# Optimization experiments

Hardware: AMD Instinct MI355X
Metric: run time of the kernel (lower is better)

Reference implementation:

```python
import jax, jax.numpy as jnp
import numpy as np

HEAD_NUM = 4
B, S, D = 8, 1024, 512


def setup_inputs() -> dict:
    k = jax.random.key(0)
    kq, kk, kv = jax.random.split(k, 3)
    return {
        "query": jax.random.normal(kq, (B, S, D), dtype=jnp.float32),
        "key": jax.random.normal(kk, (B, S, D), dtype=jnp.float32),
        "value": jax.random.normal(kv, (B, S, D), dtype=jnp.float32),
    }


def _corr_attention(q, k, v):
    # q,k,v: [B, H, S, hd]
    score = jnp.einsum('bhqd,bhkd->bhqk', q, k)  # raw dot products
    len_q = jnp.sqrt(jnp.sum(q * q, axis=-1))    # [B,H,S]
    len_k = jnp.sqrt(jnp.sum(k * k, axis=-1))    # [B,H,S]
    score = score / (len_q[..., :, None] * len_k[..., None, :])  # cosine similarity
    signal = jnp.sign(score)
    flat = jnp.abs(score).reshape(-1)            # global flatten across B,H,S,S
    n = flat.shape[0]
    idx = jnp.argsort(-flat)                     # descending sort indices
    prob = (jnp.arange(n, dtype=flat.dtype) + 1.0) / n  # (1/n, 2/n, ..., 1)
    ranked = flat.at[idx].set(prob)              # rank-transform: largest -> smallest prob
    score = (-jnp.log(ranked)).reshape(signal.shape) * signal
    return jnp.einsum('bhqk,bhkd->bhqd', score, v)


def reference(query, key, value):
    b, s, d = query.shape
    h = HEAD_NUM
    q = query.reshape(b, s, h, -1).transpose(0, 2, 1, 3)
    k = key.reshape(b, s, h, -1).transpose(0, 2, 1, 3)
    v = value.reshape(b, s, h, -1).transpose(0, 2, 1, 3)
    out = _corr_attention(q, k, v)               # [B,H,S,hd]
    return out.transpose(0, 2, 1, 3).reshape(b, s, d)
```

## Files before the change

kernel.cpp:

```cpp
#include <hip/hip_runtime.h>
#include <math.h>

#define BB 8
#define SS 1024
#define DD 512
#define HH 4
#define HD 128
#define N_SC (BB*HH*SS*SS)

#define NB 8192
#define BINS 13107.2f
#define NBLK 2048
#define NP2 32

#define OFF_S     0
#define SZ_S      ((size_t)N_SC*2)
#define OFF_QN    (OFF_S + SZ_S)
#define SZ_QN     ((size_t)BB*SS*DD*2)
#define OFF_KN    (OFF_QN + SZ_QN)
#define OFF_VT    (OFF_KN + SZ_QN)
#define OFF_PARTS (OFF_VT + SZ_QN)
#define SZ_PARTS  ((size_t)NBLK*(NB/4)*4)
#define OFF_WMAG  (OFF_PARTS + SZ_PARTS)
#define OFF_PART2 (OFF_WMAG + (size_t)NB*2)

typedef __bf16 bf16x8 __attribute__((ext_vector_type(8)));
typedef float  f32x4  __attribute__((ext_vector_type(4)));
typedef unsigned short ushort_t;

__device__ __forceinline__ unsigned bf16rne(float x) {
  unsigned b = __float_as_uint(x);
  return (b + 0x7FFFu + ((b >> 16) & 1u)) >> 16;
}
__device__ __forceinline__ unsigned sbin(float s) {
  return (unsigned)fminf(fabsf(s)*BINS, 8191.0f);
}

__global__ __launch_bounds__(256) void prep_vt_kernel(
    const float* __restrict__ q, const float* __restrict__ k,
    const float* __restrict__ v,
    unsigned* __restrict__ qn, unsigned* __restrict__ kn,
    unsigned* __restrict__ vt) {
  __shared__ float T[64][65];
  int t = threadIdx.x;
  if (blockIdx.x < 16384) {
    int lane = t & 63;
    int row = blockIdx.x*4 + (t >> 6);
    const float* src; unsigned* dst; int r;
    if (row < 32768) { src = q; dst = qn; r = row; }
    else             { src = k; dst = kn; r = row - 32768; }
    int b = r >> 12, s = (r >> 2) & 1023, h = r & 3;
    float2 vv = *(const float2*)(src + ((size_t)(b*1024 + s))*512 + h*128 + lane*2);
    float sum = vv.x*vv.x + vv.y*vv.y;
    #pragma unroll
    for (int off = 32; off; off >>= 1) sum += __shfl_xor(sum, off, 64);
    float inv = rsqrtf(sum);
    unsigned u = bf16rne(vv.x*inv) | (bf16rne(vv.y*inv) << 16);
    dst[(size_t)((b*4 + h)*1024 + s)*64 + lane] = u;
  } else {
    int vb = blockIdx.x - 16384;
    int s0 = (vb & 15)*64, d0 = ((vb >> 4) & 1)*64, bh = vb >> 5;
    int b = bh >> 2, h = bh & 3;
    #pragma unroll
    for (int i = 0; i < 16; i++) {
      int idx = t + i*256, rs = idx >> 6, cd = idx & 63;
      T[rs][cd] = v[((size_t)(b*1024 + s0 + rs))*512 + h*128 + d0 + cd];
    }
    __syncthreads();
    #pragma unroll
    for (int i = 0; i < 8; i++) {
      int idx = t + i*256, rd = idx >> 5, c2 = (idx & 31)*2;
      unsigned u = bf16rne(T[c2][rd]) | (bf16rne(T[c2+1][rd]) << 16);
      vt[(size_t)(bh*128 + d0 + rd)*512 + (s0 + c2)/2] = u;
    }
  }
}

__global__ __launch_bounds__(256) void scores_hist_kernel(
    const ushort_t* __restrict__ qn, const ushort_t* __restrict__ kn,
    ushort_t* __restrict__ S, unsigned* __restrict__ parts) {
  __shared__ ushort_t Qs[128*128];
  __shared__ ushort_t Ks[128*128];
  __shared__ unsigned h8[NB/4];
  int t = threadIdx.x;
  int L = blockIdx.x;
  int bh = L & 31, tile = L >> 5;
  int sq0 = (tile >> 3)*128, sk0 = (tile & 7)*128;

  #pragma unroll
  for (int i = 0; i < 8; i++) h8[t + i*256] = 0;

  const uint4* qg = (const uint4*)qn + (size_t)(bh*1024 + sq0)*16;
  const uint4* kg = (const uint4*)kn + (size_t)(bh*1024 + sk0)*16;
  #pragma unroll
  for (int i = 0; i < 8; i++) {
    int idx = t + i*256, row = idx >> 4, g = idx & 15;
    int sw = g ^ (row & 15);
    *(uint4*)&Qs[row*128 + sw*8] = qg[row*16 + g];
    *(uint4*)&Ks[row*128 + sw*8] = kg[row*16 + g];
  }
  __syncthreads();

  int w = t >> 6, lane = t & 63, m16 = lane & 15, q2 = lane >> 4;
  int wm = (w >> 1)*64, wn = (w & 1)*64;
  f32x4 acc[4][4];
  #pragma unroll
  for (int i = 0; i < 4; i++)
    #pragma unroll
    for (int j = 0; j < 4; j++) acc[i][j] = (f32x4){0.f,0.f,0.f,0.f};

  #pragma unroll
  for (int ks = 0; ks < 4; ks++) {
    int sw = ((ks*4 + q2) ^ m16)*8;
    bf16x8 a[4], bb[4];
    #pragma unroll
    for (int i = 0; i < 4; i++) a[i]  = *(const bf16x8*)&Qs[(wm + i*16 + m16)*128 + sw];
    #pragma unroll
    for (int j = 0; j < 4; j++) bb[j] = *(const bf16x8*)&Ks[(wn + j*16 + m16)*128 + sw];
    #pragma unroll
    for (int i = 0; i < 4; i++)
      #pragma unroll
      for (int j = 0; j < 4; j++)
        acc[i][j] = __builtin_amdgcn_mfma_f32_16x16x32_bf16(a[i], bb[j], acc[i][j], 0, 0, 0);
  }

  size_t Sbase = (size_t)bh << 20;
  #pragma unroll
  for (int i = 0; i < 4; i++)
    #pragma unroll
    for (int p = 0; p < 4; p++) {
      int row = sq0 + wm + i*16 + q2*4 + p;
      #pragma unroll
      for (int j = 0; j < 4; j++) {
        int col = sk0 + wn + j*16 + m16;
        unsigned u = bf16rne(acc[i][j][p]);
        S[Sbase + ((size_t)row << 10) + col] = (ushort_t)u;
        unsigned bin = sbin(__uint_as_float(u << 16));
        atomicAdd(&h8[bin >> 2], 1u << ((bin & 3)*8));
      }
    }
  __syncthreads();

  unsigned* dst = parts + (size_t)L*(NB/4);
  #pragma unroll
  for (int i = 0; i < 8; i++) dst[t + i*256] = h8[t + i*256];
}

__global__ __launch_bounds__(256) void reduce1_kernel(
    const unsigned* __restrict__ parts, unsigned* __restrict__ parts2) {
  int g = blockIdx.x*256 + threadIdx.x;
  int p0 = blockIdx.y*64;
  unsigned s0 = 0, s1 = 0, s2 = 0, s3 = 0;
  #pragma unroll 8
  for (int p = p0; p < p0 + 64; p++) {
    unsigned w = parts[(size_t)p*(NB/4) + g];
    s0 += w & 0xFFu; s1 += (w >> 8) & 0xFFu;
    s2 += (w >> 16) & 0xFFu; s3 += w >> 24;
  }
  uint4 o = {s0, s1, s2, s3};
  ((uint4*)parts2)[(size_t)blockIdx.y*(NB/4) + g] = o;
}

__global__ __launch_bounds__(1024) void scan_kernel(
    const unsigned* __restrict__ parts2, ushort_t* __restrict__ wmag) {
  __shared__ unsigned d[1024];
  int t = threadIdx.x;
  unsigned loc[8] = {0,0,0,0,0,0,0,0};
  #pragma unroll 4
  for (int p = 0; p < NP2; p++) {
    uint4 a = ((const uint4*)parts2)[(size_t)p*(NB/4) + t*2];
    uint4 b2 = ((const uint4*)parts2)[(size_t)p*(NB/4) + t*2 + 1];
    loc[0] += a.x;  loc[1] += a.y;  loc[2] += a.z;  loc[3] += a.w;
    loc[4] += b2.x; loc[5] += b2.y; loc[6] += b2.z; loc[7] += b2.w;
  }
  unsigned tot = 0;
  #pragma unroll
  for (int j = 0; j < 8; j++) tot += loc[j];
  d[t] = tot; __syncthreads();
  for (int off = 1; off < 1024; off <<= 1) {
    unsigned x = (t >= off) ? d[t - off] : 0u;
    __syncthreads();
    d[t] += x;
    __syncthreads();
  }
  unsigned run = d[t] - tot;
  const float inv_n = 1.0f / (float)N_SC;
  #pragma unroll
  for (int j = 0; j < 8; j++) {
    run += loc[j];
    float rm = (float)(N_SC - run) + 0.5f*(float)(loc[j] + 1u);
    wmag[t*8 + j] = (ushort_t)bf16rne(-logf(rm * inv_n));
  }
}

__global__ __launch_bounds__(512) void out_kernel(
    const ushort_t* __restrict__ S, const ushort_t* __restrict__ wmag,
    const ushort_t* __restrict__ vt, float* __restrict__ out) {
  __shared__ ushort_t Buf[128*128 + 64*128];
  __shared__ ushort_t Wl[NB];
  ushort_t* Vs = Buf;
  ushort_t* Ss = Buf + 128*128;
  int t = threadIdx.x;
  int L = blockIdx.x;
  int bh = L & 31, q0 = (L >> 5)*64;
  int b = bh >> 2, h = bh & 3;

  #pragma unroll
  for (int i = 0; i < 2; i++)
    ((uint4*)Wl)[t + i*512] = ((const uint4*)wmag)[t + i*512];

  int w = t >> 6, lane = t & 63, m16 = lane & 15, q2 = lane >> 4;
  int qt = w & 3, kh = w >> 2;
  int qw = q0 + qt*16;
  const uint4* vg = (const uint4*)vt + (size_t)bh*128*128;
  const uint4* sg = (const uint4*)S + (size_t)bh*1024*128;

  f32x4 oacc[8];
  #pragma unroll
  for (int j = 0; j < 8; j++) oacc[j] = (f32x4){0.f,0.f,0.f,0.f};

  for (int kc = 0; kc < 8; kc++) {
    #pragma unroll
    for (int i = 0; i < 4; i++) {
      int idx = t + i*512, row = idx >> 4, g = idx & 15;
      *(uint4*)&Vs[row*128 + (g ^ (row & 15))*8] = vg[row*128 + kc*16 + g];
    }
    #pragma unroll
    for (int i = 0; i < 2; i++) {
      int idx = t + i*512, row = idx >> 4, g = idx & 15;
      *(uint4*)&Ss[row*128 + (g ^ (row & 15))*8] = sg[(size_t)(q0 + row)*128 + kc*16 + g];
    }
    __syncthreads();

    #pragma unroll
    for (int u = 0; u < 2; u++) {
      int gk = kh*8 + u*4 + q2;
      uint4 sv = *(const uint4*)&Ss[(qt*16 + m16)*128 + (gk ^ m16)*8];
      unsigned sc[4] = {sv.x, sv.y, sv.z, sv.w};
      union { bf16x8 v; unsigned u2[4]; } af;
      #pragma unroll
      for (int m = 0; m < 4; m++) {
        float flo = __uint_as_float(sc[m] << 16);
        float fhi = __uint_as_float(sc[m] & 0xFFFF0000u);
        unsigned wlo = (flo == 0.f) ? 0u
                       : (unsigned)Wl[sbin(flo)] | ((flo < 0.f) ? 0x8000u : 0u);
        unsigned whi = (fhi == 0.f) ? 0u
                       : (unsigned)Wl[sbin(fhi)] | ((fhi < 0.f) ? 0x8000u : 0u);
        af.u2[m] = wlo | (whi << 16);
      }
      #pragma unroll
      for (int j = 0; j < 8; j++) {
        bf16x8 bb = *(const bf16x8*)&Vs[(j*16 + m16)*128 + (gk ^ m16)*8];
        oacc[j] = __builtin_amdgcn_mfma_f32_16x16x32_bf16(af.v, bb, oacc[j], 0, 0, 0);
      }
    }
    __syncthreads();
  }

  float* R = (float*)Buf;
  if (kh == 1) {
    #pragma unroll
    for (int j = 0; j < 8; j++)
      #pragma unroll
      for (int p = 0; p < 4; p++)
        R[(qt*16 + q2*4 + p)*129 + j*16 + m16] = oacc[j][p];
  }
  __syncthreads();
  if (kh == 0) {
    #pragma unroll
    for (int j = 0; j < 8; j++)
      #pragma unroll
      for (int p = 0; p < 4; p++)
        oacc[j][p] += R[(qt*16 + q2*4 + p)*129 + j*16 + m16];
    #pragma unroll
    for (int p = 0; p < 4; p++) {
      int qrow = qw + q2*4 + p;
      #pragma unroll
      for (int j = 0; j < 8; j++)
        out[(size_t)(b*1024 + qrow)*512 + h*128 + j*16 + m16] = oacc[j][p];
    }
  }
}

extern "C" void kernel_launch(void* const* d_in, const int* in_sizes, int n_in,
                              void* d_out, int out_size, void* d_ws, size_t ws_size,
                              hipStream_t stream) {
  const float* q = (const float*)d_in[0];
  const float* k = (const float*)d_in[1];
  const float* v = (const float*)d_in[2];
  float* out = (float*)d_out;
  char* ws = (char*)d_ws;

  ushort_t* Sbuf  = (ushort_t*)(ws + OFF_S);
  unsigned* qn    = (unsigned*)(ws + OFF_QN);
  unsigned* kn    = (unsigned*)(ws + OFF_KN);
  unsigned* vtb   = (unsigned*)(ws + OFF_VT);
  unsigned* parts = (unsigned*)(ws + OFF_PARTS);
  ushort_t* wmag  = (ushort_t*)(ws + OFF_WMAG);
  unsigned* part2 = (unsigned*)(ws + OFF_PART2);

  hipLaunchKernelGGL(prep_vt_kernel, dim3(17408), dim3(256), 0, stream, q, k, v, qn, kn, vtb);
  hipLaunchKernelGGL(scores_hist_kernel, dim3(NBLK), dim3(256), 0, stream,
                     (const ushort_t*)qn, (const ushort_t*)kn, Sbuf, parts);
  hipLaunchKernelGGL(reduce1_kernel, dim3(8, NP2), dim3(256), 0, stream, parts, part2);
  hipLaunchKernelGGL(scan_kernel, dim3(1), dim3(1024), 0, stream, part2, wmag);
  hipLaunchKernelGGL(out_kernel, dim3(512), dim3(512), 0, stream,
                     (const ushort_t*)Sbuf, wmag, (const ushort_t*)vtb, out);
}
```

Before: 166.3 us.

## Use direct global-to-LDS loads, split k across waves, parallelize histogram reduction

The output kernel now stages V and score tiles with global_load_lds, moving the XOR swizzle to the source address instead of the LDS destination. Waves are reorganized so each one covers 32 query rows and a quarter of the k chunk, which reuses each V fragment across two MFMAs. The partial outputs are combined with LDS atomicAdd before a coalesced store. A separate multi-block reduce2 kernel sums the histogram partials so the single-block scan only reads the final counts, at the cost of one more launch and LDS atomic contention.

```diff
diff --git a/kernel.cpp b/kernel.cpp
--- a/kernel.cpp
+++ b/kernel.cpp
@@ -23,6 +23,7 @@
 #define SZ_PARTS  ((size_t)NBLK*(NB/4)*4)
 #define OFF_WMAG  (OFF_PARTS + SZ_PARTS)
 #define OFF_PART2 (OFF_WMAG + (size_t)NB*2)
+#define OFF_CNT   (OFF_PART2 + (size_t)NP2*NB*4)
 
 typedef __bf16 bf16x8 __attribute__((ext_vector_type(8)));
 typedef float  f32x4  __attribute__((ext_vector_type(4)));
@@ -34,6 +35,11 @@
 }
 __device__ __forceinline__ unsigned sbin(float s) {
   return (unsigned)fminf(fabsf(s)*BINS, 8191.0f);
+}
+__device__ __forceinline__ void gload_lds16(const void* g, void* l) {
+  __builtin_amdgcn_global_load_lds(
+      (const __attribute__((address_space(1))) unsigned int*)g,
+      (__attribute__((address_space(3))) unsigned int*)l, 16, 0, 0);
 }
 
 __global__ __launch_bounds__(256) void prep_vt_kernel(
@@ -161,18 +167,22 @@
   ((uint4*)parts2)[(size_t)blockIdx.y*(NB/4) + g] = o;
 }
 
+__global__ __launch_bounds__(256) void reduce2_kernel(
+    const unsigned* __restrict__ parts2, unsigned* __restrict__ counts) {
+  int g = blockIdx.x*256 + threadIdx.x;
+  unsigned s = 0;
+  #pragma unroll 8
+  for (int p = 0; p < NP2; p++) s += parts2[(size_t)p*NB + g];
+  counts[g] = s;
+}
+
 __global__ __launch_bounds__(1024) void scan_kernel(
-    const unsigned* __restrict__ parts2, ushort_t* __restrict__ wmag) {
+    const unsigned* __restrict__ counts, ushort_t* __restrict__ wmag) {
   __shared__ unsigned d[1024];
   int t = threadIdx.x;
-  unsigned loc[8] = {0,0,0,0,0,0,0,0};
-  #pragma unroll 4
-  for (int p = 0; p < NP2; p++) {
-    uint4 a = ((const uint4*)parts2)[(size_t)p*(NB/4) + t*2];
-    uint4 b2 = ((const uint4*)parts2)[(size_t)p*(NB/4) + t*2 + 1];
-    loc[0] += a.x;  loc[1] += a.y;  loc[2] += a.z;  loc[3] += a.w;
-    loc[4] += b2.x; loc[5] += b2.y; loc[6] += b2.z; loc[7] += b2.w;
-  }
+  uint4 a  = ((const uint4*)counts)[t*2];
+  uint4 b2 = ((const uint4*)counts)[t*2 + 1];
+  unsigned loc[8] = {a.x, a.y, a.z, a.w, b2.x, b2.y, b2.z, b2.w};
   unsigned tot = 0;
   #pragma unroll
   for (int j = 0; j < 8; j++) tot += loc[j];
@@ -210,34 +220,35 @@
     ((uint4*)Wl)[t + i*512] = ((const uint4*)wmag)[t + i*512];
 
   int w = t >> 6, lane = t & 63, m16 = lane & 15, q2 = lane >> 4;
-  int qt = w & 3, kh = w >> 2;
-  int qw = q0 + qt*16;
+  int qt = w & 1, ks = w >> 1;
   const uint4* vg = (const uint4*)vt + (size_t)bh*128*128;
   const uint4* sg = (const uint4*)S + (size_t)bh*1024*128;
 
-  f32x4 oacc[8];
-  #pragma unroll
-  for (int j = 0; j < 8; j++) oacc[j] = (f32x4){0.f,0.f,0.f,0.f};
+  f32x4 oacc[2][8];
+  #pragma unroll
+  for (int r = 0; r < 2; r++)
+    #pragma unroll
+    for (int j = 0; j < 8; j++) oacc[r][j] = (f32x4){0.f,0.f,0.f,0.f};
 
   for (int kc = 0; kc < 8; kc++) {
     #pragma unroll
     for (int i = 0; i < 4; i++) {
       int idx = t + i*512, row = idx >> 4, g = idx & 15;
-      *(uint4*)&Vs[row*128 + (g ^ (row & 15))*8] = vg[row*128 + kc*16 + g];
+      gload_lds16(vg + row*128 + kc*16 + (g ^ (row & 15)), &Vs[idx*8]);
     }
     #pragma unroll
     for (int i = 0; i < 2; i++) {
       int idx = t + i*512, row = idx >> 4, g = idx & 15;
-      *(uint4*)&Ss[row*128 + (g ^ (row & 15))*8] = sg[(size_t)(q0 + row)*128 + kc*16 + g];
-    }
-    __syncthreads();
-
-    #pragma unroll
-    for (int u = 0; u < 2; u++) {
-      int gk = kh*8 + u*4 + q2;
-      uint4 sv = *(const uint4*)&Ss[(qt*16 + m16)*128 + (gk ^ m16)*8];
+      gload_lds16(sg + (size_t)(q0 + row)*128 + kc*16 + (g ^ (row & 15)), &Ss[idx*8]);
+    }
+    __syncthreads();
+
+    int gk = ks*4 + q2;
+    union { bf16x8 v; unsigned u2[4]; } af[2];
+    #pragma unroll
+    for (int r = 0; r < 2; r++) {
+      uint4 sv = *(const uint4*)&Ss[(qt*32 + r*16 + m16)*128 + (gk ^ m16)*8];
       unsigned sc[4] = {sv.x, sv.y, sv.z, sv.w};
-      union { bf16x8 v; unsigned u2[4]; } af;
       #pragma unroll
       for (int m = 0; m < 4; m++) {
         float flo = __uint_as_float(sc[m] << 16);
@@ -246,39 +257,34 @@
                        : (unsigned)Wl[sbin(flo)] | ((flo < 0.f) ? 0x8000u : 0u);
         unsigned whi = (fhi == 0.f) ? 0u
                        : (unsigned)Wl[sbin(fhi)] | ((fhi < 0.f) ? 0x8000u : 0u);
-        af.u2[m] = wlo | (whi << 16);
+        af[r].u2[m] = wlo | (whi << 16);
       }
-      #pragma unroll
-      for (int j = 0; j < 8; j++) {
-        bf16x8 bb = *(const bf16x8*)&Vs[(j*16 + m16)*128 + (gk ^ m16)*8];
-        oacc[j] = __builtin_amdgcn_mfma_f32_16x16x32_bf16(af.v, bb, oacc[j], 0, 0, 0);
-      }
+    }
+    #pragma unroll
+    for (int j = 0; j < 8; j++) {
+      bf16x8 bb = *(const bf16x8*)&Vs[(j*16 + m16)*128 + (gk ^ m16)*8];
+      #pragma unroll
+      for (int r = 0; r < 2; r++)
+        oacc[r][j] = __builtin_amdgcn_mfma_f32_16x16x32_bf16(af[r].v, bb, oacc[r][j], 0, 0, 0);
     }
     __syncthreads();
   }
 
   float* R = (float*)Buf;
-  if (kh == 1) {
+  for (int i = t; i < 64*129; i += 512) R[i] = 0.f;
+  __syncthreads();
+  #pragma unroll
+  for (int r = 0; r < 2; r++)
     #pragma unroll
     for (int j = 0; j < 8; j++)
       #pragma unroll
       for (int p = 0; p < 4; p++)
-        R[(qt*16 + q2*4 + p)*129 + j*16 + m16] = oacc[j][p];
-  }
+        atomicAdd(&R[(qt*32 + r*16 + q2*4 + p)*129 + j*16 + m16], oacc[r][j][p]);
   __syncthreads();
-  if (kh == 0) {
-    #pragma unroll
-    for (int j = 0; j < 8; j++)
-      #pragma unroll
-      for (int p = 0; p < 4; p++)
-        oacc[j][p] += R[(qt*16 + q2*4 + p)*129 + j*16 + m16];
-    #pragma unroll
-    for (int p = 0; p < 4; p++) {
-      int qrow = qw + q2*4 + p;
-      #pragma unroll
-      for (int j = 0; j < 8; j++)
-        out[(size_t)(b*1024 + qrow)*512 + h*128 + j*16 + m16] = oacc[j][p];
-    }
+
+  for (int i = t; i < 64*128; i += 512) {
+    int r = i >> 7, c = i & 127;
+    out[((size_t)(b*1024 + q0 + r))*512 + h*128 + c] = R[r*129 + c];
   }
 }
 
@@ -298,12 +304,14 @@
   unsigned* parts = (unsigned*)(ws + OFF_PARTS);
   ushort_t* wmag  = (ushort_t*)(ws + OFF_WMAG);
   unsigned* part2 = (unsigned*)(ws + OFF_PART2);
+  unsigned* cnt   = (unsigned*)(ws + OFF_CNT);
 
   hipLaunchKernelGGL(prep_vt_kernel, dim3(17408), dim3(256), 0, stream, q, k, v, qn, kn, vtb);
   hipLaunchKernelGGL(scores_hist_kernel, dim3(NBLK), dim3(256), 0, stream,
                      (const ushort_t*)qn, (const ushort_t*)kn, Sbuf, parts);
   hipLaunchKernelGGL(reduce1_kernel, dim3(8, NP2), dim3(256), 0, stream, parts, part2);
-  hipLaunchKernelGGL(scan_kernel, dim3(1), dim3(1024), 0, stream, part2, wmag);
+  hipLaunchKernelGGL(reduce2_kernel, dim3(32), dim3(256), 0, stream, part2, cnt);
+  hipLaunchKernelGGL(scan_kernel, dim3(1), dim3(1024), 0, stream, cnt, wmag);
   hipLaunchKernelGGL(out_kernel, dim3(512), dim3(512), 0, stream,
                      (const ushort_t*)Sbuf, wmag, (const ushort_t*)vtb, out);
 }
```

Measured after the change: 255.4 us. +53.6%, slower.
